# Optimization experiments

Hardware: AMD Instinct MI355X
Metric: run time of the kernel (lower is better)

## Reference

```python
import jax, jax.numpy as jnp
import numpy as np

N = 33554432          # flat genome length (multiple of chunk_size -> no padding)
CS = 64               # chunk_size
REF = 16              # ref_dim
HID = 64              # hidden
SPLIT = N // 2        # weight_coords[0]: policy/meta split index


def setup_inputs() -> dict:
    key = jax.random.key(0)
    ks = jax.random.split(key, 12)
    nc = N // CS
    rn = lambda k, shape, sc=1.0: jax.random.normal(k, shape, dtype=jnp.float32) * sc
    return {
        "flat_weights": rn(ks[0], (N,)),
        "other_weights": rn(ks[1], (N,)),
        "weight_coords": jnp.array([SPLIT], dtype=jnp.int32),
        "noise": rn(ks[2], (nc, CS)),                      # unit gaussian, scaled inside
        "w_enc": rn(ks[3], (REF, CS), 0.1),
        "b_enc": jnp.zeros((REF,), jnp.float32),
        "w_c1": rn(ks[4], (HID, 3 * REF), 0.1),
        "b_c1": jnp.zeros((HID,), jnp.float32),
        "w_c2": rn(ks[5], (CS, HID), 0.1),
        "b_c2": jnp.zeros((CS,), jnp.float32),
        "w_g1": rn(ks[6], (HID, 4 * REF), 0.1),
        "b_g1": jnp.zeros((HID,), jnp.float32),
        "w_g2": rn(ks[7], (2, HID), 0.1),
        "b_g2": jnp.zeros((2,), jnp.float32),
        "ref_policy": rn(ks[8], (REF,), 0.1),
        "ref_meta": rn(ks[9], (REF,), 0.1),
        "cs_policy": jnp.array(0.03, jnp.float32),
        "cs_meta": jnp.array(0.01, jnp.float32),
        "es_policy": jnp.array(0.01, jnp.float32),
        "es_meta": jnp.array(0.002, jnp.float32),
    }


def _encode(x, w_enc, b_enc):
    # nn.Sequential(Linear(CS->REF), Tanh())
    return jnp.tanh(x @ w_enc.T + b_enc)


def reference(flat_weights, other_weights, weight_coords, noise,
              w_enc, b_enc, w_c1, b_c1, w_c2, b_c2,
              w_g1, b_g1, w_g2, b_g2,
              ref_policy, ref_meta, cs_policy, cs_meta, es_policy, es_meta):
    split = weight_coords[0]
    a = flat_weights.reshape(-1, CS)     # [nc, CS]
    b = other_weights.reshape(-1, CS)    # [nc, CS]

    # ---- gated crossover blend (sigmoid mode, clamp = 0) ----
    ea = _encode(a, w_enc, b_enc)
    eb = _encode(b, w_enc, b_enc)
    gate_in = jnp.concatenate([ea, eb, ea - eb, ea * eb], axis=1)  # [nc, 4*REF]
    logits = jnp.tanh(gate_in @ w_g1.T + b_g1) @ w_g2.T + b_g2     # [nc, 2]
    alpha = jax.nn.sigmoid(logits[:, 0] - logits[:, 1])[:, None]   # [nc, 1]
    base = alpha * a + (1.0 - alpha) * b

    # ---- dual-head (policy/meta) masked correction ----
    nc = base.shape[0]
    mask = (jnp.arange(nc, dtype=jnp.int32) * CS < split)[:, None]  # True -> policy
    enc = _encode(base, w_enc, b_enc)                               # [nc, REF]
    ref = jnp.where(mask, ref_policy, ref_meta)                     # [nc, REF]
    x = jnp.concatenate([enc, ref, enc - ref], axis=1)              # [nc, 3*REF]
    corr = jnp.tanh(jnp.tanh(x @ w_c1.T + b_c1) @ w_c2.T + b_c2)    # [nc, CS]
    corr = jnp.clip(corr * jnp.where(mask, cs_policy, cs_meta), -0.1, 0.1)

    # ---- masked exploration noise ----
    mutated = base + corr + noise * jnp.where(mask, es_policy, es_meta)
    return mutated.reshape(-1)[:N]
```

## Files before the change

kernel.cpp:

```cpp
#include <hip/hip_runtime.h>
#include <math.h>

#define NTOT 33554432
#define CS 64
#define REF 16
#define HID 64
#define NC (NTOT / CS)

typedef float fx4 __attribute__((ext_vector_type(4)));

#define WS_FLOATS 9409

#if defined(__has_builtin)
#if __has_builtin(__builtin_amdgcn_rcpf)
#define FAST_RCP(x) __builtin_amdgcn_rcpf(x)
#endif
#endif
#ifndef FAST_RCP
#define FAST_RCP(x) (1.0f / (x))
#endif

__device__ __forceinline__ float fast_tanh(float x) {
  float e = __expf(2.0f * x);
  return 1.0f - 2.0f * FAST_RCP(e + 1.0f);
}

__device__ __forceinline__ float get4(const float4& v, int c) {
  return c == 0 ? v.x : c == 1 ? v.y : c == 2 ? v.z : v.w;
}

__global__ void setup_fold_kernel(const float* __restrict__ w_g1,
                                  const float* __restrict__ w_c1,
                                  const float* __restrict__ b_c1,
                                  const float* __restrict__ w_enc,
                                  const float* __restrict__ w_c2,
                                  const float* __restrict__ w_g2,
                                  const float* __restrict__ b_g2,
                                  const float* __restrict__ ref_p,
                                  const float* __restrict__ ref_m,
                                  float* __restrict__ ws) {
  const int t = threadIdx.x;
  for (int idx = t; idx < 1024; idx += 256) {
    const int j = idx >> 4, k = idx & 15;
    ws[idx]        = w_g1[j * 64 + k] + w_g1[j * 64 + 32 + k];
    ws[1024 + idx] = w_g1[j * 64 + 16 + k] - w_g1[j * 64 + 32 + k];
    ws[2048 + idx] = w_g1[j * 64 + 48 + k];
    ws[3072 + idx] = w_c1[j * 48 + k] + w_c1[j * 48 + 32 + k];
    ws[8320 + idx] = w_enc[(idx & 15) * 64 + (idx >> 4)];
  }
  for (int idx = t; idx < 4096; idx += 256) {
    const int j = idx >> 6, i = idx & 63;
    ws[4224 + idx] = w_c2[i * 64 + j];
  }
  if (t < 64) {
    float sp = b_c1[t], sm = b_c1[t];
    for (int k = 0; k < REF; ++k) {
      const float wd = w_c1[t * 48 + 16 + k] - w_c1[t * 48 + 32 + k];
      sp += ref_p[k] * wd;
      sm += ref_m[k] * wd;
    }
    ws[4096 + t] = sp;
    ws[4160 + t] = sm;
    ws[9344 + t] = w_g2[t] - w_g2[64 + t];
  }
  if (t == 0) ws[9408] = b_g2[0] - b_g2[1];
}

__global__ void __launch_bounds__(256) dual_mutate_kernel(
    const float* __restrict__ A, const float* __restrict__ B,
    const int* __restrict__ coords, const float* __restrict__ noise,
    const float* __restrict__ b_enc, const float* __restrict__ b_c2,
    const float* __restrict__ b_g1,
    const float* __restrict__ cs_p, const float* __restrict__ cs_m,
    const float* __restrict__ es_p, const float* __restrict__ es_m,
    const float* __restrict__ ws, float* __restrict__ out) {
  const int chunk = blockIdx.x * blockDim.x + threadIdx.x;
  if (chunk >= NC) return;
  const size_t off = (size_t)chunk * CS;
  const float* ap = A + off;
  const float* bp = B + off;

  float za[REF], zb[REF];
#pragma unroll
  for (int j = 0; j < REF; ++j) {
    const float bj = b_enc[j];
    za[j] = bj;
    zb[j] = bj;
  }
#pragma unroll 4
  for (int k4 = 0; k4 < CS / 4; ++k4) {
    const float4 a4 = *reinterpret_cast<const float4*>(ap + 4 * k4);
    const float4 b4 = *reinterpret_cast<const float4*>(bp + 4 * k4);
#pragma unroll
    for (int c = 0; c < 4; ++c) {
      const float av = get4(a4, c);
      const float bv = get4(b4, c);
      const int k = 4 * k4 + c;
      const float* wT = ws + 8320 + k * REF;
#pragma unroll
      for (int j = 0; j < REF; ++j) {
        za[j] = fmaf(av, wT[j], za[j]);
        zb[j] = fmaf(bv, wT[j], zb[j]);
      }
    }
  }

  float ea[REF], eb[REF], pp[REF];
#pragma unroll
  for (int j = 0; j < REF; ++j) {
    ea[j] = fast_tanh(za[j]);
    eb[j] = fast_tanh(zb[j]);
    pp[j] = ea[j] * eb[j];
  }
  float logit = ws[9408];
#pragma unroll 2
  for (int j = 0; j < HID; ++j) {
    float acc = b_g1[j];
#pragma unroll
    for (int k = 0; k < REF; ++k) {
      acc = fmaf(ea[k], ws[j * REF + k], acc);
      acc = fmaf(eb[k], ws[1024 + j * REF + k], acc);
      acc = fmaf(pp[k], ws[2048 + j * REF + k], acc);
    }
    logit = fmaf(ws[9344 + j], fast_tanh(acc), logit);
  }
  const float alpha = FAST_RCP(1.0f + __expf(-logit));

  const int split = coords[0];
  const bool policy = (chunk * CS) < split;
  float enc[REF];
#pragma unroll
  for (int j = 0; j < REF; ++j)
    enc[j] = fast_tanh(fmaf(alpha, za[j] - zb[j], zb[j]));

  const float csv = policy ? cs_p[0] : cs_m[0];
  const float esv = policy ? es_p[0] : es_m[0];
  const float* np_ = noise + off;
  float* op = out + off;

#pragma unroll 1
  for (int s = 0; s < 2; ++s) {
    float corrA[16], corrB[16];
#pragma unroll
    for (int ii = 0; ii < 16; ++ii) {
      corrA[ii] = b_c2[s * 32 + ii];
      corrB[ii] = b_c2[s * 32 + 16 + ii];
    }
#pragma unroll 2
    for (int j = 0; j < HID; ++j) {
      const float c0p = ws[4096 + j];
      const float c0m = ws[4160 + j];
      float acc = policy ? c0p : c0m;
      const float* wc = ws + 3072 + j * REF;
#pragma unroll
      for (int k = 0; k < REF; ++k) acc = fmaf(enc[k], wc[k], acc);
      const float hj = fast_tanh(acc);
      const float* w2 = ws + 4224 + j * HID + s * 32;
#pragma unroll
      for (int ii = 0; ii < 16; ++ii) corrA[ii] = fmaf(hj, w2[ii], corrA[ii]);
#pragma unroll
      for (int ii = 0; ii < 16; ++ii) corrB[ii] = fmaf(hj, w2[16 + ii], corrB[ii]);
    }
#pragma unroll
    for (int q = 0; q < 8; ++q) {
      const int i0 = s * 32 + 4 * q;
      const float4 a4 = *reinterpret_cast<const float4*>(ap + i0);
      const float4 b4 = *reinterpret_cast<const float4*>(bp + i0);
      const fx4 n4 = __builtin_nontemporal_load(
          reinterpret_cast<const fx4*>(np_ + i0));
      fx4 o;
#pragma unroll
      for (int c = 0; c < 4; ++c) {
        const float av = get4(a4, c);
        const float bv = get4(b4, c);
        const float bb = fmaf(alpha, av - bv, bv);
        const float cr = (q < 4) ? ((const float*)corrA)[(4 * q + c) & 15]
                                 : ((const float*)corrB)[(4 * q + c) & 15];
        float cv = fast_tanh(cr) * csv;
        cv = fminf(fmaxf(cv, -0.1f), 0.1f);
        o[c] = bb + cv + n4[c] * esv;
      }
      __builtin_nontemporal_store(o, reinterpret_cast<fx4*>(op + i0));
    }
  }
}

extern "C" void kernel_launch(void* const* d_in, const int* in_sizes, int n_in,
                              void* d_out, int out_size, void* d_ws, size_t ws_size,
                              hipStream_t stream) {
  const float* A     = (const float*)d_in[0];
  const float* B     = (const float*)d_in[1];
  const int*   coord = (const int*)d_in[2];
  const float* noise = (const float*)d_in[3];
  const float* w_enc = (const float*)d_in[4];
  const float* b_enc = (const float*)d_in[5];
  const float* w_c1  = (const float*)d_in[6];
  const float* b_c1  = (const float*)d_in[7];
  const float* w_c2  = (const float*)d_in[8];
  const float* b_c2  = (const float*)d_in[9];
  const float* w_g1  = (const float*)d_in[10];
  const float* b_g1  = (const float*)d_in[11];
  const float* w_g2  = (const float*)d_in[12];
  const float* b_g2  = (const float*)d_in[13];
  const float* ref_p = (const float*)d_in[14];
  const float* ref_m = (const float*)d_in[15];
  const float* cs_p  = (const float*)d_in[16];
  const float* cs_m  = (const float*)d_in[17];
  const float* es_p  = (const float*)d_in[18];
  const float* es_m  = (const float*)d_in[19];
  float* out = (float*)d_out;
  float* ws  = (float*)d_ws;

  setup_fold_kernel<<<1, 256, 0, stream>>>(w_g1, w_c1, b_c1, w_enc, w_c2,
                                           w_g2, b_g2, ref_p, ref_m, ws);

  const int blocks = NC / 256;
  dual_mutate_kernel<<<blocks, 256, 0, stream>>>(
      A, B, coord, noise, b_enc, b_c2, b_g1,
      cs_p, cs_m, es_p, es_m, ws, out);
}
```

Baseline: 494.6 us.

## Compute hidden layer once and cache it in LDS as bf16

```diff
diff --git a/kernel.cpp b/kernel.cpp
--- a/kernel.cpp
+++ b/kernel.cpp
@@ -8,6 +8,7 @@
 #define NC (NTOT / CS)
 
 typedef float fx4 __attribute__((ext_vector_type(4)));
+typedef unsigned ux4 __attribute__((ext_vector_type(4)));
 
 #define WS_FLOATS 9409
 
@@ -27,6 +28,18 @@
 
 __device__ __forceinline__ float get4(const float4& v, int c) {
   return c == 0 ? v.x : c == 1 ? v.y : c == 2 ? v.z : v.w;
+}
+
+__device__ __forceinline__ unsigned bpack2(float lo, float hi) {
+  unsigned ul = __builtin_bit_cast(unsigned, lo);
+  unsigned uh = __builtin_bit_cast(unsigned, hi);
+  return ((ul + 0x8000u) >> 16) | ((uh + 0x8000u) & 0xFFFF0000u);
+}
+__device__ __forceinline__ float blo(unsigned p) {
+  return __builtin_bit_cast(float, p << 16);
+}
+__device__ __forceinline__ float bhi(unsigned p) {
+  return __builtin_bit_cast(float, p & 0xFFFF0000u);
 }
 
 __global__ void setup_fold_kernel(const float* __restrict__ w_g1,
@@ -74,7 +87,11 @@
     const float* __restrict__ cs_p, const float* __restrict__ cs_m,
     const float* __restrict__ es_p, const float* __restrict__ es_m,
     const float* __restrict__ ws, float* __restrict__ out) {
-  const int chunk = blockIdx.x * blockDim.x + threadIdx.x;
+  __shared__ unsigned lds_u[256 * 36];
+  const int tid = threadIdx.x;
+  unsigned* row = lds_u + tid * 36;
+
+  const int chunk = blockIdx.x * blockDim.x + tid;
   if (chunk >= NC) return;
   const size_t off = (size_t)chunk * CS;
   const float* ap = A + off;
@@ -105,13 +122,20 @@
     }
   }
 
-  float ea[REF], eb[REF], pp[REF];
+#pragma unroll
+  for (int q = 0; q < 4; ++q) {
+    ux4 p;
+#pragma unroll
+    for (int m = 0; m < 4; ++m) p[m] = bpack2(za[4 * q + m], zb[4 * q + m]);
+    *reinterpret_cast<ux4*>(row + 4 * q) = p;
+  }
+  float ea[REF], eb[REF];
 #pragma unroll
   for (int j = 0; j < REF; ++j) {
     ea[j] = fast_tanh(za[j]);
     eb[j] = fast_tanh(zb[j]);
-    pp[j] = ea[j] * eb[j];
-  }
+  }
+
   float logit = ws[9408];
 #pragma unroll 2
   for (int j = 0; j < HID; ++j) {
@@ -120,7 +144,7 @@
     for (int k = 0; k < REF; ++k) {
       acc = fmaf(ea[k], ws[j * REF + k], acc);
       acc = fmaf(eb[k], ws[1024 + j * REF + k], acc);
-      acc = fmaf(pp[k], ws[2048 + j * REF + k], acc);
+      acc = fmaf(ea[k] * eb[k], ws[2048 + j * REF + k], acc);
     }
     logit = fmaf(ws[9344 + j], fast_tanh(acc), logit);
   }
@@ -130,40 +154,63 @@
   const bool policy = (chunk * CS) < split;
   float enc[REF];
 #pragma unroll
-  for (int j = 0; j < REF; ++j)
-    enc[j] = fast_tanh(fmaf(alpha, za[j] - zb[j], zb[j]));
+  for (int q = 0; q < 4; ++q) {
+    const ux4 p = *reinterpret_cast<const ux4*>(row + 4 * q);
+#pragma unroll
+    for (int m = 0; m < 4; ++m) {
+      const float zav = blo(p[m]);
+      const float zbv = bhi(p[m]);
+      enc[4 * q + m] = fast_tanh(fmaf(alpha, zav - zbv, zbv));
+    }
+  }
+
+#pragma unroll 1
+  for (int jo = 0; jo < 8; ++jo) {
+    float hv[8];
+#pragma unroll
+    for (int c = 0; c < 8; ++c) {
+      const int j = jo * 8 + c;
+      float acc = policy ? ws[4096 + j] : ws[4160 + j];
+      const float* wc = ws + 3072 + j * REF;
+#pragma unroll
+      for (int k = 0; k < REF; ++k) acc = fmaf(enc[k], wc[k], acc);
+      hv[c] = fast_tanh(acc);
+    }
+    ux4 p;
+#pragma unroll
+    for (int m = 0; m < 4; ++m) p[m] = bpack2(hv[2 * m], hv[2 * m + 1]);
+    *reinterpret_cast<ux4*>(row + 4 * jo) = p;
+  }
 
   const float csv = policy ? cs_p[0] : cs_m[0];
   const float esv = policy ? es_p[0] : es_m[0];
   const float* np_ = noise + off;
   float* op = out + off;
-
 #pragma unroll 1
-  for (int s = 0; s < 2; ++s) {
-    float corrA[16], corrB[16];
-#pragma unroll
-    for (int ii = 0; ii < 16; ++ii) {
-      corrA[ii] = b_c2[s * 32 + ii];
-      corrB[ii] = b_c2[s * 32 + 16 + ii];
-    }
-#pragma unroll 2
-    for (int j = 0; j < HID; ++j) {
-      const float c0p = ws[4096 + j];
-      const float c0m = ws[4160 + j];
-      float acc = policy ? c0p : c0m;
-      const float* wc = ws + 3072 + j * REF;
-#pragma unroll
-      for (int k = 0; k < REF; ++k) acc = fmaf(enc[k], wc[k], acc);
-      const float hj = fast_tanh(acc);
-      const float* w2 = ws + 4224 + j * HID + s * 32;
-#pragma unroll
-      for (int ii = 0; ii < 16; ++ii) corrA[ii] = fmaf(hj, w2[ii], corrA[ii]);
-#pragma unroll
-      for (int ii = 0; ii < 16; ++ii) corrB[ii] = fmaf(hj, w2[16 + ii], corrB[ii]);
-    }
-#pragma unroll
-    for (int q = 0; q < 8; ++q) {
-      const int i0 = s * 32 + 4 * q;
+  for (int s = 0; s < 4; ++s) {
+    float corr[16];
+#pragma unroll
+    for (int ii = 0; ii < 16; ++ii) corr[ii] = b_c2[s * 16 + ii];
+#pragma unroll 1
+    for (int jo = 0; jo < 8; ++jo) {
+      const ux4 p = *reinterpret_cast<const ux4*>(row + 4 * jo);
+      float hf[8];
+#pragma unroll
+      for (int m = 0; m < 4; ++m) {
+        hf[2 * m] = blo(p[m]);
+        hf[2 * m + 1] = bhi(p[m]);
+      }
+      const float* w2 = ws + 4224 + (jo * 8) * HID + s * 16;
+#pragma unroll
+      for (int c = 0; c < 8; ++c) {
+#pragma unroll
+        for (int ii = 0; ii < 16; ++ii)
+          corr[ii] = fmaf(hf[c], w2[c * HID + ii], corr[ii]);
+      }
+    }
+#pragma unroll
+    for (int q = 0; q < 4; ++q) {
+      const int i0 = s * 16 + 4 * q;
       const float4 a4 = *reinterpret_cast<const float4*>(ap + i0);
       const float4 b4 = *reinterpret_cast<const float4*>(bp + i0);
       const fx4 n4 = __builtin_nontemporal_load(
@@ -174,9 +221,7 @@
         const float av = get4(a4, c);
         const float bv = get4(b4, c);
         const float bb = fmaf(alpha, av - bv, bv);
-        const float cr = (q < 4) ? ((const float*)corrA)[(4 * q + c) & 15]
-                                 : ((const float*)corrB)[(4 * q + c) & 15];
-        float cv = fast_tanh(cr) * csv;
+        float cv = fast_tanh(corr[4 * q + c]) * csv;
         cv = fminf(fmaxf(cv, -0.1f), 0.1f);
         o[c] = bb + cv + n4[c] * esv;
       }
```

Result: faster. 471.5 us (-4.7%).
